# Kernel tuning notes

Measured on AMD Instinct MI355X. Metric: run time of the kernel, lower is better.

The kernel has to match this reference:

```python
import jax, jax.numpy as jnp
import numpy as np

BATCH = 64
ORIGINAL_DIM = 524288
PROJ_DIM = 8192
C = 4


def setup_inputs() -> dict:
    key = jax.random.key(0)
    k1, k2, k3 = jax.random.split(key, 3)
    x = jax.random.normal(k1, (BATCH, ORIGINAL_DIM), dtype=jnp.float32)
    rand_indices = jax.random.randint(k2, (ORIGINAL_DIM, C), 0, PROJ_DIM, dtype=jnp.int32)
    rand_signs = jax.random.randint(k3, (ORIGINAL_DIM, C), 0, 2, dtype=jnp.int32)
    return {"x": x, "rand_indices": rand_indices, "rand_signs": rand_signs}


def reference(x, rand_indices, rand_signs):
    # SJLT: out[b, rand_indices[d, j]] += x[b, d] * sign[d, j], scaled by 1/sqrt(c)
    B, D = x.shape
    c = rand_indices.shape[1]
    signs = (2 * rand_signs - 1).astype(x.dtype)  # {0,1} -> {-1,+1}
    scale = 1.0 / jnp.sqrt(jnp.asarray(c, dtype=x.dtype))
    out = jnp.zeros((B, PROJ_DIM), dtype=x.dtype)
    for j in range(c):  # small fixed loop over non-zeros per column
        out = out.at[:, rand_indices[:, j]].add(x * signs[:, j])
    return out * scale
```

## Files before the change

kernel.cpp:

```cpp
#include <hip/hip_runtime.h>


constexpr int BATCH = 64;
constexpr int DIM   = 524288;
constexpr int PROJ  = 8192;
constexpr int NENT  = DIM * 4;
constexpr int CAP   = 384;

constexpr int NBLKA = 256;
constexpr int EPB   = NENT / NBLKA;
constexpr int NBUCK = 256;
constexpr int BUCKP = PROJ / NBUCK;
constexpr int CAPB  = 80;

__device__ __forceinline__ uint32_t f2bf(float f) {
    uint32_t u = __float_as_uint(f);
    return (u + 0x7fffu + ((u >> 16) & 1u)) >> 16;
}

__global__ __launch_bounds__(256) void transpose_kernel(
    const float* __restrict__ x, uint32_t* __restrict__ xT)
{
    __shared__ float tile[64][65];
    const int d0 = blockIdx.x * 64;
    const int t  = threadIdx.x;

    const int c  = t & 15;
    const int r0 = t >> 4;
    float4 v[4];
#pragma unroll
    for (int it = 0; it < 4; ++it) {
        int b = it * 16 + r0;
        v[it] = *reinterpret_cast<const float4*>(&x[(size_t)b * DIM + d0 + 4 * c]);
    }
#pragma unroll
    for (int it = 0; it < 4; ++it) {
        int b = it * 16 + r0;
        tile[b][4 * c + 0] = v[it].x;
        tile[b][4 * c + 1] = v[it].y;
        tile[b][4 * c + 2] = v[it].z;
        tile[b][4 * c + 3] = v[it].w;
    }
    __syncthreads();

    const int a  = t & 7;
    const int dr = t >> 3;
#pragma unroll
    for (int pass = 0; pass < 2; ++pass) {
        const int dl = pass * 32 + dr;
        uint4 wv;
        uint32_t* wq = reinterpret_cast<uint32_t*>(&wv);
#pragma unroll
        for (int q = 0; q < 4; ++q) {
            const int k = 4 * a + q;
            uint32_t lo = f2bf(tile[2 * k + 0][dl] * 0.5f);
            uint32_t hi = f2bf(tile[2 * k + 1][dl] * 0.5f);
            wq[q] = lo | (hi << 16);
        }
        *reinterpret_cast<uint4*>(&xT[(size_t)(d0 + dl) * 32 + 4 * a]) = wv;
    }
}

__global__ __launch_bounds__(1024) void binA_kernel(
    const int4* __restrict__ idx4, const int4* __restrict__ sgn4,
    uint32_t* __restrict__ cntAB, uint32_t* __restrict__ coarse)
{
    __shared__ uint32_t cntL[NBUCK], offL[NBUCK], curL[NBUCK];
    __shared__ uint32_t wsumA[4];
    __shared__ uint32_t staging[EPB];
    const int t    = threadIdx.x;
    const int lane = t & 63;
    const int blk  = blockIdx.x;

    if (t < NBUCK) cntL[t] = 0;
    __syncthreads();

    int4 iv[2], sv[2];
    int  dd[2];
#pragma unroll
    for (int j = 0; j < 2; ++j) {
        int d = blk * 2048 + j * 1024 + t;
        dd[j] = d;
        iv[j] = idx4[d];
        sv[j] = sgn4[d];
    }
#pragma unroll
    for (int j = 0; j < 2; ++j) {
        atomicAdd(&cntL[(uint32_t)iv[j].x >> 5], 1u);
        atomicAdd(&cntL[(uint32_t)iv[j].y >> 5], 1u);
        atomicAdd(&cntL[(uint32_t)iv[j].z >> 5], 1u);
        atomicAdd(&cntL[(uint32_t)iv[j].w >> 5], 1u);
    }
    __syncthreads();
    uint32_t v = 0, s = 0;
    if (t < NBUCK) {
        s = cntL[t]; v = s;
#pragma unroll
        for (int off = 1; off < 64; off <<= 1) {
            uint32_t u = __shfl_up(v, off);
            if (lane >= off) v += u;
        }
        if (lane == 63) wsumA[t >> 6] = v;
    }
    __syncthreads();
    if (t < NBUCK) {
        uint32_t wb = 0;
        for (int w0 = 0; w0 < (t >> 6); ++w0) wb += wsumA[w0];
        uint32_t ex = wb + v - s;
        offL[t] = ex;
        curL[t] = ex;
    }
    __syncthreads();
#pragma unroll
    for (int j = 0; j < 2; ++j) {
        const uint32_t dv = (uint32_t)dd[j] << 1;
        int p, ss;
        uint32_t b, sl;
        p = iv[j].x; ss = sv[j].x & 1; b = (uint32_t)p >> 5;
        sl = atomicAdd(&curL[b], 1u);
        staging[sl] = ((uint32_t)(p & 31) << 20) | dv | (uint32_t)ss;
        p = iv[j].y; ss = sv[j].y & 1; b = (uint32_t)p >> 5;
        sl = atomicAdd(&curL[b], 1u);
        staging[sl] = ((uint32_t)(p & 31) << 20) | dv | (uint32_t)ss;
        p = iv[j].z; ss = sv[j].z & 1; b = (uint32_t)p >> 5;
        sl = atomicAdd(&curL[b], 1u);
        staging[sl] = ((uint32_t)(p & 31) << 20) | dv | (uint32_t)ss;
        p = iv[j].w; ss = sv[j].w & 1; b = (uint32_t)p >> 5;
        sl = atomicAdd(&curL[b], 1u);
        staging[sl] = ((uint32_t)(p & 31) << 20) | dv | (uint32_t)ss;
    }
    __syncthreads();
    const int w = t >> 6;
    for (int i = 0; i < NBUCK / 16; ++i) {
        const int b = w * (NBUCK / 16) + i;
        const uint32_t c   = min(cntL[b], (uint32_t)CAPB);
        const uint32_t src = offL[b];
        uint32_t* dst = coarse + ((size_t)b * NBLKA + blk) * CAPB;
        for (uint32_t j2 = lane; j2 < c; j2 += 64) dst[j2] = staging[src + j2];
    }
    if (t < NBUCK) cntAB[(size_t)blk * NBUCK + t] = min(cntL[t], (uint32_t)CAPB);
}

__global__ __launch_bounds__(1024) void gather6_kernel(
    const uint32_t* __restrict__ coarse, const uint32_t* __restrict__ cntAB,
    const uint32_t* __restrict__ xT, float* __restrict__ out)
{
    __shared__ uint32_t csr[16 * CAP];
    __shared__ uint32_t cntF[16];
    __shared__ uint32_t cAB[NBLKA];
    __shared__ float    obuf[64][17];
    const int t       = threadIdx.x;
    const int w       = t >> 6;
    const int lane    = t & 63;
    const int bucket  = blockIdx.x >> 1;
    const int halfsel = blockIdx.x & 1;

    if (t < 16) cntF[t] = 0;
    if (t < NBLKA) cAB[t] = cntAB[(size_t)t * NBUCK + bucket];
    __syncthreads();

    const int hw = t >> 5;
    const int l  = t & 31;
    for (int i = 0; i < NBLKA / 32; ++i) {
        const int j = hw * (NBLKA / 32) + i;
        const uint32_t c = cAB[j];
        const uint32_t* src = coarse + ((size_t)bucket * NBLKA + j) * CAPB;
        for (uint32_t i2 = l; i2 < c; i2 += 32) {
            const uint32_t pay = src[i2];
            const uint32_t pg  = (pay >> 20) & 31u;
            if ((int)(pg >> 4) == halfsel) {
                const uint32_t pl = pg & 15u;
                const uint32_t sl = atomicAdd(&cntF[pl], 1u);
                csr[pl * CAP + sl] = pay & 0xFFFFFu;
            }
        }
    }
    __syncthreads();

    const int half = lane >> 5;
    const int k    = lane & 31;
    const uint32_t n = cntF[w];
    const uint32_t* e = &csr[w * CAP];
    float acc0 = 0.f, acc1 = 0.f;
    uint32_t base = 0;
    for (; base + 8 <= n; base += 8) {
        uint32_t e8[8];
#pragma unroll
        for (int q = 0; q < 8; ++q) e8[q] = e[base + q];
#pragma unroll
        for (int q = 0; q < 8; q += 2) {
            uint32_t sel = half ? e8[q + 1] : e8[q];
            uint32_t u = xT[(size_t)(sel >> 1) * 32 + k];
            u ^= (sel & 1u) ? 0u : 0x80008000u;
            acc0 += __uint_as_float(u << 16);
            acc1 += __uint_as_float(u & 0xffff0000u);
        }
    }
    for (; base < n; base += 2) {
        uint32_t eA = e[base];
        uint32_t eB = (base + 1 < n) ? e[base + 1] : 0u;
        uint32_t sel   = half ? eB : eA;
        bool     valid = (base + (uint32_t)half) < n;
        uint32_t u = 0u;
        if (valid) {
            u = xT[(size_t)(sel >> 1) * 32 + k];
            u ^= (sel & 1u) ? 0u : 0x80008000u;
        }
        acc0 += __uint_as_float(u << 16);
        acc1 += __uint_as_float(u & 0xffff0000u);
    }
    acc0 += __shfl_xor(acc0, 32);
    acc1 += __shfl_xor(acc1, 32);
    if (half == 0) {
        obuf[2 * k + 0][w] = acc0;
        obuf[2 * k + 1][w] = acc1;
    }
    __syncthreads();
    if (t < 256) {
        const int b = t >> 2, q = t & 3;
        float4 vv;
        vv.x = obuf[b][4 * q + 0];
        vv.y = obuf[b][4 * q + 1];
        vv.z = obuf[b][4 * q + 2];
        vv.w = obuf[b][4 * q + 3];
        *reinterpret_cast<float4*>(
            &out[(size_t)b * PROJ + bucket * BUCKP + halfsel * 16 + 4 * q]) = vv;
    }
}

__global__ __launch_bounds__(256) void fused_tx_scatter(
    const float* __restrict__ x, const int* __restrict__ idx,
    const int* __restrict__ sgn, uint32_t* __restrict__ cnt,
    uint32_t* __restrict__ entries, uint32_t* __restrict__ xT)
{
    __shared__ float tile[64][65];
    const int d0 = blockIdx.x * 64;
    const int t  = threadIdx.x;

    const int e = (d0 << 2) + t;
    const int p = idx[e];
    const int s = sgn[e] & 1;

    const int c  = t & 15;
    const int r0 = t >> 4;
    float4 v[4];
#pragma unroll
    for (int it = 0; it < 4; ++it) {
        int b = it * 16 + r0;
        v[it] = *reinterpret_cast<const float4*>(&x[(size_t)b * DIM + d0 + 4 * c]);
    }
    {
        uint32_t dv   = ((uint32_t)(d0 + (t >> 2)) << 1) | (uint32_t)s;
        uint32_t slot = atomicAdd(&cnt[p], 1u);
        entries[(uint32_t)p * (uint32_t)CAP + slot] = dv;
    }
#pragma unroll
    for (int it = 0; it < 4; ++it) {
        int b = it * 16 + r0;
        tile[b][4 * c + 0] = v[it].x;
        tile[b][4 * c + 1] = v[it].y;
        tile[b][4 * c + 2] = v[it].z;
        tile[b][4 * c + 3] = v[it].w;
    }
    __syncthreads();
    const int a  = t & 7;
    const int dr = t >> 3;
#pragma unroll
    for (int pass = 0; pass < 2; ++pass) {
        const int dl = pass * 32 + dr;
        uint4 wv;
        uint32_t* wq = reinterpret_cast<uint32_t*>(&wv);
#pragma unroll
        for (int q = 0; q < 4; ++q) {
            const int k = 4 * a + q;
            uint32_t lo = f2bf(tile[2 * k + 0][dl] * 0.5f);
            uint32_t hi = f2bf(tile[2 * k + 1][dl] * 0.5f);
            wq[q] = lo | (hi << 16);
        }
        *reinterpret_cast<uint4*>(&xT[(size_t)(d0 + dl) * 32 + 4 * a]) = wv;
    }
}

__device__ __forceinline__ void proc8(const uint32_t* __restrict__ e,
    const uint32_t* __restrict__ xT, int half, int k,
    float& acc0, float& acc1)
{
#pragma unroll
    for (int t = 0; t < 8; t += 2) {
        uint32_t sel = half ? e[t + 1] : e[t];
        uint32_t u = xT[(size_t)(sel >> 1) * 32 + k];
        u ^= (sel & 1u) ? 0u : 0x80008000u;
        acc0 += __uint_as_float(u << 16);
        acc1 += __uint_as_float(u & 0xffff0000u);
    }
}

__global__ __launch_bounds__(1024) void gather4_kernel(
    const uint32_t* __restrict__ entries, const uint32_t* __restrict__ cnt,
    const uint32_t* __restrict__ xT, float* __restrict__ out)
{
    __shared__ float obuf[64][17];
    const int w    = threadIdx.x >> 6;
    const int lane = threadIdx.x & 63;
    const int p    = __builtin_amdgcn_readfirstlane(blockIdx.x * 16 + w);
    const uint32_t n  = __builtin_amdgcn_readfirstlane(cnt[p]);
    const uint32_t e0 = (uint32_t)p * (uint32_t)CAP;

    const int half = lane >> 5;
    const int k    = lane & 31;
    float acc0 = 0.f, acc1 = 0.f;

    uint32_t A[8], B[8];
    uint32_t base = 0;
    if (n >= 8) {
#pragma unroll
        for (int t = 0; t < 8; ++t) A[t] = entries[e0 + t];
    }
    for (; base + 24 <= n; base += 16) {
#pragma unroll
        for (int t = 0; t < 8; ++t) B[t] = entries[e0 + base + 8 + t];
        proc8(A, xT, half, k, acc0, acc1);
#pragma unroll
        for (int t = 0; t < 8; ++t) A[t] = entries[e0 + base + 16 + t];
        proc8(B, xT, half, k, acc0, acc1);
    }
    if (base + 16 <= n) {
#pragma unroll
        for (int t = 0; t < 8; ++t) B[t] = entries[e0 + base + 8 + t];
        proc8(A, xT, half, k, acc0, acc1);
        proc8(B, xT, half, k, acc0, acc1);
        base += 16;
    } else if (base + 8 <= n) {
        proc8(A, xT, half, k, acc0, acc1);
        base += 8;
    }
    for (; base < n; base += 2) {
        uint32_t eA = entries[e0 + base];
        uint32_t eB = (base + 1 < n) ? entries[e0 + base + 1] : 0u;
        uint32_t sel   = half ? eB : eA;
        bool     valid = (base + (uint32_t)half) < n;
        uint32_t u = 0u;
        if (valid) {
            u = xT[(size_t)(sel >> 1) * 32 + k];
            u ^= (sel & 1u) ? 0u : 0x80008000u;
        }
        acc0 += __uint_as_float(u << 16);
        acc1 += __uint_as_float(u & 0xffff0000u);
    }
    acc0 += __shfl_xor(acc0, 32);
    acc1 += __shfl_xor(acc1, 32);
    if (half == 0) {
        obuf[2 * k + 0][w] = acc0;
        obuf[2 * k + 1][w] = acc1;
    }
    __syncthreads();
    const int t = threadIdx.x;
    if (t < 256) {
        const int b = t >> 2, q = t & 3;
        float4 v;
        v.x = obuf[b][4 * q + 0];
        v.y = obuf[b][4 * q + 1];
        v.z = obuf[b][4 * q + 2];
        v.w = obuf[b][4 * q + 3];
        *reinterpret_cast<float4*>(&out[(size_t)b * PROJ + blockIdx.x * 16 + 4 * q]) = v;
    }
}

__device__ __forceinline__ void lds_fadd(uint32_t byte_addr, float v) {
    asm volatile("ds_add_f32 %0, %1" :: "v"(byte_addr), "v"(v) : "memory");
}
__device__ __forceinline__ void lds_fadd_off32k(uint32_t byte_addr, float v) {
    asm volatile("ds_add_f32 %0, %1 offset:32768" :: "v"(byte_addr), "v"(v) : "memory");
}

__global__ __launch_bounds__(1024) void sjlt_scatter(
    const float* __restrict__ x, const int4* __restrict__ idx4,
    const int4* __restrict__ sgn4, float* __restrict__ out)
{
    __shared__ float acc[4 * PROJ];
    for (int i = threadIdx.x; i < 4 * PROJ; i += 1024) acc[i] = 0.0f;
    __syncthreads();
    const int row0 = blockIdx.y * 4;
    const int dbeg = blockIdx.x * (DIM / 16);
    const uint32_t accBase = (uint32_t)(uintptr_t)(&acc[0]);
    const float* xr0 = x + (size_t)(row0 + 0) * DIM;
    const float* xr1 = x + (size_t)(row0 + 1) * DIM;
    const float* xr2 = x + (size_t)(row0 + 2) * DIM;
    const float* xr3 = x + (size_t)(row0 + 3) * DIM;
    for (int d = dbeg + (int)threadIdx.x; d < dbeg + DIM / 16; d += 1024) {
        const int4 iv = idx4[d];
        const int4 sv = sgn4[d];
        const uint32_t u0 = __float_as_uint(xr0[d]);
        const uint32_t u1 = __float_as_uint(xr1[d]);
        const uint32_t u2 = __float_as_uint(xr2[d]);
        const uint32_t u3 = __float_as_uint(xr3[d]);
        const int p[4] = {iv.x, iv.y, iv.z, iv.w};
        const int s[4] = {sv.x, sv.y, sv.z, sv.w};
#pragma unroll
        for (int j = 0; j < 4; ++j) {
            const uint32_t flip = (uint32_t)(s[j] ^ 1) << 31;
            const uint32_t a01  = accBase + ((uint32_t)p[j] << 2);
            const uint32_t a23  = a01 + 2u * 32768u;
            lds_fadd        (a01, __uint_as_float(u0 ^ flip));
            lds_fadd_off32k (a01, __uint_as_float(u1 ^ flip));
            lds_fadd        (a23, __uint_as_float(u2 ^ flip));
            lds_fadd_off32k (a23, __uint_as_float(u3 ^ flip));
        }
    }
    __syncthreads();
    for (int i = threadIdx.x; i < 4 * PROJ; i += 1024) {
        const int r  = i >> 13;
        const int pp = i & (PROJ - 1);
        unsafeAtomicAdd(&out[(size_t)(row0 + r) * PROJ + pp], acc[i] * 0.5f);
    }
}

extern "C" void kernel_launch(void* const* d_in, const int* in_sizes, int n_in,
                              void* d_out, int out_size, void* d_ws, size_t ws_size,
                              hipStream_t stream) {
    const float* x   = (const float*)d_in[0];
    const int4*  idx = (const int4*) d_in[1];
    const int4*  sgn = (const int4*) d_in[2];
    float*       out = (float*)d_out;

    const size_t need_r11 = ((size_t)NBLKA * NBUCK
                           + (size_t)NBUCK * NBLKA * CAPB
                           + (size_t)DIM * 32) * 4;
    const size_t need_r9  = ((size_t)PROJ + (size_t)PROJ * CAP + (size_t)DIM * 32) * 4;

    if (ws_size >= need_r11) {
        uint32_t* cntAB  = (uint32_t*)d_ws;
        uint32_t* coarse = cntAB + (size_t)NBLKA * NBUCK;
        uint32_t* xT     = coarse + (size_t)NBUCK * NBLKA * CAPB;

        transpose_kernel<<<DIM / 64,  256, 0, stream>>>(x, xT);
        binA_kernel     <<<NBLKA,     1024, 0, stream>>>(idx, sgn, cntAB, coarse);
        gather6_kernel  <<<NBUCK * 2, 1024, 0, stream>>>(coarse, cntAB, xT, out);
    } else if (ws_size >= need_r9) {
        uint32_t* cnt     = (uint32_t*)d_ws;
        uint32_t* entries = cnt + PROJ;
        uint32_t* xT      = entries + (size_t)PROJ * CAP;

        hipMemsetAsync(cnt, 0, PROJ * sizeof(uint32_t), stream);
        fused_tx_scatter<<<DIM / 64, 256, 0, stream>>>(
            x, (const int*)idx, (const int*)sgn, cnt, entries, xT);
        gather4_kernel<<<PROJ / 16, 1024, 0, stream>>>(entries, cnt, xT, out);
    } else {
        hipMemsetAsync(d_out, 0, (size_t)out_size * sizeof(float), stream);
        dim3 grid(16, 16);
        sjlt_scatter<<<grid, 1024, 0, stream>>>(x, idx, sgn, out);
    }
}
```

Before: 305.5 us.

## Fuse transpose and binning into one heterogeneous prep kernel, pad CSR stride

Result: slower. 318.0 us (+4.1%).

```diff
diff --git a/kernel.cpp b/kernel.cpp
--- a/kernel.cpp
+++ b/kernel.cpp
@@ -6,146 +6,141 @@
 constexpr int PROJ  = 8192;
 constexpr int NENT  = DIM * 4;
 constexpr int CAP   = 384;
+constexpr int CSTR  = 385;
 
 constexpr int NBLKA = 256;
 constexpr int EPB   = NENT / NBLKA;
 constexpr int NBUCK = 256;
 constexpr int BUCKP = PROJ / NBUCK;
 constexpr int CAPB  = 80;
+constexpr int TBLK  = 2048;
 
 __device__ __forceinline__ uint32_t f2bf(float f) {
     uint32_t u = __float_as_uint(f);
     return (u + 0x7fffu + ((u >> 16) & 1u)) >> 16;
 }
 
-__global__ __launch_bounds__(256) void transpose_kernel(
-    const float* __restrict__ x, uint32_t* __restrict__ xT)
-{
-    __shared__ float tile[64][65];
-    const int d0 = blockIdx.x * 64;
-    const int t  = threadIdx.x;
-
-    const int c  = t & 15;
-    const int r0 = t >> 4;
-    float4 v[4];
-#pragma unroll
-    for (int it = 0; it < 4; ++it) {
-        int b = it * 16 + r0;
-        v[it] = *reinterpret_cast<const float4*>(&x[(size_t)b * DIM + d0 + 4 * c]);
-    }
-#pragma unroll
-    for (int it = 0; it < 4; ++it) {
-        int b = it * 16 + r0;
-        tile[b][4 * c + 0] = v[it].x;
-        tile[b][4 * c + 1] = v[it].y;
-        tile[b][4 * c + 2] = v[it].z;
-        tile[b][4 * c + 3] = v[it].w;
-    }
-    __syncthreads();
-
-    const int a  = t & 7;
-    const int dr = t >> 3;
-#pragma unroll
-    for (int pass = 0; pass < 2; ++pass) {
-        const int dl = pass * 32 + dr;
-        uint4 wv;
-        uint32_t* wq = reinterpret_cast<uint32_t*>(&wv);
-#pragma unroll
-        for (int q = 0; q < 4; ++q) {
-            const int k = 4 * a + q;
-            uint32_t lo = f2bf(tile[2 * k + 0][dl] * 0.5f);
-            uint32_t hi = f2bf(tile[2 * k + 1][dl] * 0.5f);
-            wq[q] = lo | (hi << 16);
-        }
-        *reinterpret_cast<uint4*>(&xT[(size_t)(d0 + dl) * 32 + 4 * a]) = wv;
-    }
-}
-
-__global__ __launch_bounds__(1024) void binA_kernel(
-    const int4* __restrict__ idx4, const int4* __restrict__ sgn4,
-    uint32_t* __restrict__ cntAB, uint32_t* __restrict__ coarse)
-{
-    __shared__ uint32_t cntL[NBUCK], offL[NBUCK], curL[NBUCK];
-    __shared__ uint32_t wsumA[4];
-    __shared__ uint32_t staging[EPB];
-    const int t    = threadIdx.x;
-    const int lane = t & 63;
-    const int blk  = blockIdx.x;
-
-    if (t < NBUCK) cntL[t] = 0;
-    __syncthreads();
-
-    int4 iv[2], sv[2];
-    int  dd[2];
-#pragma unroll
-    for (int j = 0; j < 2; ++j) {
-        int d = blk * 2048 + j * 1024 + t;
-        dd[j] = d;
-        iv[j] = idx4[d];
-        sv[j] = sgn4[d];
-    }
-#pragma unroll
-    for (int j = 0; j < 2; ++j) {
-        atomicAdd(&cntL[(uint32_t)iv[j].x >> 5], 1u);
-        atomicAdd(&cntL[(uint32_t)iv[j].y >> 5], 1u);
-        atomicAdd(&cntL[(uint32_t)iv[j].z >> 5], 1u);
-        atomicAdd(&cntL[(uint32_t)iv[j].w >> 5], 1u);
-    }
-    __syncthreads();
-    uint32_t v = 0, s = 0;
-    if (t < NBUCK) {
-        s = cntL[t]; v = s;
-#pragma unroll
-        for (int off = 1; off < 64; off <<= 1) {
-            uint32_t u = __shfl_up(v, off);
-            if (lane >= off) v += u;
-        }
-        if (lane == 63) wsumA[t >> 6] = v;
-    }
-    __syncthreads();
-    if (t < NBUCK) {
-        uint32_t wb = 0;
-        for (int w0 = 0; w0 < (t >> 6); ++w0) wb += wsumA[w0];
-        uint32_t ex = wb + v - s;
-        offL[t] = ex;
-        curL[t] = ex;
-    }
-    __syncthreads();
-#pragma unroll
-    for (int j = 0; j < 2; ++j) {
-        const uint32_t dv = (uint32_t)dd[j] << 1;
-        int p, ss;
-        uint32_t b, sl;
-        p = iv[j].x; ss = sv[j].x & 1; b = (uint32_t)p >> 5;
-        sl = atomicAdd(&curL[b], 1u);
-        staging[sl] = ((uint32_t)(p & 31) << 20) | dv | (uint32_t)ss;
-        p = iv[j].y; ss = sv[j].y & 1; b = (uint32_t)p >> 5;
-        sl = atomicAdd(&curL[b], 1u);
-        staging[sl] = ((uint32_t)(p & 31) << 20) | dv | (uint32_t)ss;
-        p = iv[j].z; ss = sv[j].z & 1; b = (uint32_t)p >> 5;
-        sl = atomicAdd(&curL[b], 1u);
-        staging[sl] = ((uint32_t)(p & 31) << 20) | dv | (uint32_t)ss;
-        p = iv[j].w; ss = sv[j].w & 1; b = (uint32_t)p >> 5;
-        sl = atomicAdd(&curL[b], 1u);
-        staging[sl] = ((uint32_t)(p & 31) << 20) | dv | (uint32_t)ss;
-    }
-    __syncthreads();
-    const int w = t >> 6;
-    for (int i = 0; i < NBUCK / 16; ++i) {
-        const int b = w * (NBUCK / 16) + i;
-        const uint32_t c   = min(cntL[b], (uint32_t)CAPB);
-        const uint32_t src = offL[b];
-        uint32_t* dst = coarse + ((size_t)b * NBLKA + blk) * CAPB;
-        for (uint32_t j2 = lane; j2 < c; j2 += 64) dst[j2] = staging[src + j2];
-    }
-    if (t < NBUCK) cntAB[(size_t)blk * NBUCK + t] = min(cntL[t], (uint32_t)CAPB);
-}
-
-__global__ __launch_bounds__(1024) void gather6_kernel(
+__global__ __launch_bounds__(1024) void prep_kernel(
+    const float* __restrict__ x, const int4* __restrict__ idx4,
+    const int4* __restrict__ sgn4, uint32_t* __restrict__ cntAB,
+    uint32_t* __restrict__ coarse, uint32_t* __restrict__ xT)
+{
+    __shared__ uint32_t sh[8964];
+    const int t = threadIdx.x;
+
+    if (blockIdx.x < NBLKA) {
+        uint32_t* cntL    = sh;
+        uint32_t* offL    = sh + 256;
+        uint32_t* curL    = sh + 512;
+        uint32_t* wsumA   = sh + 768;
+        uint32_t* staging = sh + 772;
+        const int lane = t & 63;
+        const int blk  = blockIdx.x;
+
+        if (t < NBUCK) cntL[t] = 0;
+        __syncthreads();
+
+        int4 iv[2], sv[2];
+        int  dd[2];
+#pragma unroll
+        for (int j = 0; j < 2; ++j) {
+            int d = blk * 2048 + j * 1024 + t;
+            dd[j] = d;
+            iv[j] = idx4[d];
+            sv[j] = sgn4[d];
+        }
+#pragma unroll
+        for (int j = 0; j < 2; ++j) {
+            atomicAdd(&cntL[(uint32_t)iv[j].x >> 5], 1u);
+            atomicAdd(&cntL[(uint32_t)iv[j].y >> 5], 1u);
+            atomicAdd(&cntL[(uint32_t)iv[j].z >> 5], 1u);
+            atomicAdd(&cntL[(uint32_t)iv[j].w >> 5], 1u);
+        }
+        __syncthreads();
+        uint32_t v = 0, s = 0;
+        if (t < NBUCK) {
+            s = cntL[t]; v = s;
+#pragma unroll
+            for (int off = 1; off < 64; off <<= 1) {
+                uint32_t u = __shfl_up(v, off);
+                if (lane >= off) v += u;
+            }
+            if (lane == 63) wsumA[t >> 6] = v;
+        }
+        __syncthreads();
+        if (t < NBUCK) {
+            uint32_t wb = 0;
+            for (int w0 = 0; w0 < (t >> 6); ++w0) wb += wsumA[w0];
+            uint32_t ex = wb + v - s;
+            offL[t] = ex;
+            curL[t] = ex;
+        }
+        __syncthreads();
+#pragma unroll
+        for (int j = 0; j < 2; ++j) {
+            const uint32_t dv = (uint32_t)dd[j] << 1;
+            int p, ss;
+            uint32_t b, sl;
+            p = iv[j].x; ss = sv[j].x & 1; b = (uint32_t)p >> 5;
+            sl = atomicAdd(&curL[b], 1u);
+            staging[sl] = ((uint32_t)(p & 31) << 20) | dv | (uint32_t)ss;
+            p = iv[j].y; ss = sv[j].y & 1; b = (uint32_t)p >> 5;
+            sl = atomicAdd(&curL[b], 1u);
+            staging[sl] = ((uint32_t)(p & 31) << 20) | dv | (uint32_t)ss;
+            p = iv[j].z; ss = sv[j].z & 1; b = (uint32_t)p >> 5;
+            sl = atomicAdd(&curL[b], 1u);
+            staging[sl] = ((uint32_t)(p & 31) << 20) | dv | (uint32_t)ss;
+            p = iv[j].w; ss = sv[j].w & 1; b = (uint32_t)p >> 5;
+            sl = atomicAdd(&curL[b], 1u);
+            staging[sl] = ((uint32_t)(p & 31) << 20) | dv | (uint32_t)ss;
+        }
+        __syncthreads();
+        const int w = t >> 6;
+        for (int i = 0; i < NBUCK / 16; ++i) {
+            const int b = w * (NBUCK / 16) + i;
+            const uint32_t c   = min(cntL[b], (uint32_t)CAPB);
+            const uint32_t src = offL[b];
+            uint32_t* dst = coarse + ((size_t)b * NBLKA + blk) * CAPB;
+            for (uint32_t j2 = lane; j2 < c; j2 += 64) dst[j2] = staging[src + j2];
+        }
+        if (t < NBUCK) cntAB[(size_t)blk * NBUCK + t] = min(cntL[t], (uint32_t)CAPB);
+    } else {
+        float* tile = reinterpret_cast<float*>(sh);
+        const int blk   = blockIdx.x - NBLKA;
+        const int dbase = blk * 256;
+        const int c  = t & 15;
+        const int r  = t >> 4;
+        const int a  = t & 15;
+        const int dr = t >> 4;
+#pragma unroll
+        for (int it = 0; it < 4; ++it) {
+            const int d0 = dbase + it * 64;
+            float4 v = *reinterpret_cast<const float4*>(
+                &x[(size_t)r * DIM + d0 + 4 * c]);
+            __syncthreads();
+            tile[r * 65 + 4 * c + 0] = v.x;
+            tile[r * 65 + 4 * c + 1] = v.y;
+            tile[r * 65 + 4 * c + 2] = v.z;
+            tile[r * 65 + 4 * c + 3] = v.w;
+            __syncthreads();
+            uint32_t lo, hi;
+            lo = f2bf(tile[(4 * a + 0) * 65 + dr] * 0.5f);
+            hi = f2bf(tile[(4 * a + 1) * 65 + dr] * 0.5f);
+            const uint32_t w0 = lo | (hi << 16);
+            lo = f2bf(tile[(4 * a + 2) * 65 + dr] * 0.5f);
+            hi = f2bf(tile[(4 * a + 3) * 65 + dr] * 0.5f);
+            const uint32_t w1 = lo | (hi << 16);
+            uint2 wv; wv.x = w0; wv.y = w1;
+            *reinterpret_cast<uint2*>(&xT[(size_t)(d0 + dr) * 32 + 2 * a]) = wv;
+        }
+    }
+}
+
+__global__ __launch_bounds__(1024) void gather7_kernel(
     const uint32_t* __restrict__ coarse, const uint32_t* __restrict__ cntAB,
     const uint32_t* __restrict__ xT, float* __restrict__ out)
 {
-    __shared__ uint32_t csr[16 * CAP];
+    __shared__ uint32_t csr[16 * CSTR];
     __shared__ uint32_t cntF[16];
     __shared__ uint32_t cAB[NBLKA];
     __shared__ float    obuf[64][17];
@@ -171,7 +166,7 @@
             if ((int)(pg >> 4) == halfsel) {
                 const uint32_t pl = pg & 15u;
                 const uint32_t sl = atomicAdd(&cntF[pl], 1u);
-                csr[pl * CAP + sl] = pay & 0xFFFFFu;
+                csr[pl * CSTR + sl] = pay & 0xFFFFFu;
             }
         }
     }
@@ -180,7 +175,7 @@
     const int half = lane >> 5;
     const int k    = lane & 31;
     const uint32_t n = cntF[w];
-    const uint32_t* e = &csr[w * CAP];
+    const uint32_t* e = &csr[w * CSTR];
     float acc0 = 0.f, acc1 = 0.f;
     uint32_t base = 0;
     for (; base + 8 <= n; base += 8) {
@@ -423,19 +418,19 @@
     const int4*  sgn = (const int4*) d_in[2];
     float*       out = (float*)d_out;
 
-    const size_t need_r11 = ((size_t)NBLKA * NBUCK
+    const size_t need_r12 = ((size_t)NBLKA * NBUCK
                            + (size_t)NBUCK * NBLKA * CAPB
                            + (size_t)DIM * 32) * 4;
     const size_t need_r9  = ((size_t)PROJ + (size_t)PROJ * CAP + (size_t)DIM * 32) * 4;
 
-    if (ws_size >= need_r11) {
+    if (ws_size >= need_r12) {
         uint32_t* cntAB  = (uint32_t*)d_ws;
         uint32_t* coarse = cntAB + (size_t)NBLKA * NBUCK;
         uint32_t* xT     = coarse + (size_t)NBUCK * NBLKA * CAPB;
 
-        transpose_kernel<<<DIM / 64,  256, 0, stream>>>(x, xT);
-        binA_kernel     <<<NBLKA,     1024, 0, stream>>>(idx, sgn, cntAB, coarse);
-        gather6_kernel  <<<NBUCK * 2, 1024, 0, stream>>>(coarse, cntAB, xT, out);
+        prep_kernel   <<<NBLKA + TBLK, 1024, 0, stream>>>(
+            x, idx, sgn, cntAB, coarse, xT);
+        gather7_kernel<<<NBUCK * 2,    1024, 0, stream>>>(coarse, cntAB, xT, out);
     } else if (ws_size >= need_r9) {
         uint32_t* cnt     = (uint32_t*)d_ws;
         uint32_t* entries = cnt + PROJ;
```
